# Kernel tuning notes

Hardware: AMD Instinct MI355X
Metric: run time of the kernel (lower is better)

Reference implementation:

```python
import jax, jax.numpy as jnp
import numpy as np

H, NH, NKV, HD, S, B = 4096, 32, 8, 128, 2048, 1
QMAX = 127.0  # int8 symmetric


def fake_quant(x, axis=None):
    """Symmetric int8 fake quantization with straight-through estimator.
    axis=None -> per-tensor dynamic scale; axis=int -> per-channel along that axis."""
    if axis is None:
        amax = jnp.max(jnp.abs(x))
    else:
        amax = jnp.max(jnp.abs(x), axis=axis, keepdims=True)
    scale = jnp.maximum(amax, 1e-8) / QMAX
    q = jnp.clip(jnp.round(x / scale), -QMAX - 1, QMAX) * scale
    return x + jax.lax.stop_gradient(q - x)


def quant_linear(x, w):
    # weight: per-output-channel quant (reduce over in-features axis=1);
    # activation: per-tensor dynamic quant
    xq = fake_quant(x)
    wq = fake_quant(w, axis=1)
    return jnp.einsum('bsh,oh->bso', xq, wq)


def rotate_half(x):
    x1, x2 = jnp.split(x, 2, axis=-1)
    return jnp.concatenate([-x2, x1], axis=-1)


def apply_rope(q, k, cos, sin):
    # q: [B,NH,S,HD], k: [B,NKV,S,HD], cos/sin: [B,S,HD]
    cos = cos[:, None, :, :]
    sin = sin[:, None, :, :]
    return q * cos + rotate_half(q) * sin, k * cos + rotate_half(k) * sin


def setup_inputs() -> dict:
    key = jax.random.key(0)
    ks = jax.random.split(key, 6)
    hidden_states = jax.random.normal(ks[0], (B, S, H), jnp.float32)
    # additive causal mask
    neg = jnp.finfo(jnp.float32).min
    mask = jnp.where(jnp.tril(jnp.ones((S, S), bool)), 0.0, neg)
    attention_mask = jnp.broadcast_to(mask, (B, 1, S, S)).astype(jnp.float32)
    # rotary cos/sin
    inv_freq = 1.0 / (10000.0 ** (jnp.arange(0, HD, 2, dtype=jnp.float32) / HD))
    t = jnp.arange(S, dtype=jnp.float32)
    freqs = jnp.outer(t, inv_freq)                     # [S, HD/2]
    emb = jnp.concatenate([freqs, freqs], axis=-1)     # [S, HD]
    cos = jnp.broadcast_to(jnp.cos(emb), (B, S, HD))
    sin = jnp.broadcast_to(jnp.sin(emb), (B, S, HD))
    sc = 0.02
    wq = jax.random.normal(ks[1], (H, H), jnp.float32) * sc
    wk = jax.random.normal(ks[2], (NKV * HD, H), jnp.float32) * sc
    wv = jax.random.normal(ks[3], (NKV * HD, H), jnp.float32) * sc
    wo = jax.random.normal(ks[4], (H, H), jnp.float32) * sc
    return {"hidden_states": hidden_states, "attention_mask": attention_mask,
            "cos": cos, "sin": sin, "wq": wq, "wk": wk, "wv": wv, "wo": wo}


def reference(hidden_states, attention_mask, cos, sin, wq, wk, wv, wo):
    b, s, _ = hidden_states.shape
    scaling = HD ** -0.5
    q = quant_linear(hidden_states, wq).reshape(b, s, NH, HD).transpose(0, 2, 1, 3)
    k = quant_linear(hidden_states, wk).reshape(b, s, NKV, HD).transpose(0, 2, 1, 3)
    v = quant_linear(hidden_states, wv).reshape(b, s, NKV, HD).transpose(0, 2, 1, 3)
    q, k = apply_rope(q, k, cos, sin)
    groups = NH // NKV
    k = jnp.repeat(k, groups, axis=1)  # [B,NH,S,HD]
    v = jnp.repeat(v, groups, axis=1)
    # quantize before QK^T
    qq = fake_quant(q)
    kq = fake_quant(k)
    attn = jnp.einsum('bhqd,bhkd->bhqk', qq, kq) * scaling
    attn = attn + attention_mask
    attn = jnp.maximum(attn, jnp.finfo(attn.dtype).min)
    attn = jax.nn.softmax(attn.astype(jnp.float32), axis=-1).astype(q.dtype)
    # quantize before PV
    pq = fake_quant(attn)
    vq = fake_quant(v)
    out = jnp.einsum('bhqk,bhkd->bhqd', pq, vq)
    out = out.transpose(0, 2, 1, 3).reshape(b, s, NH * HD)
    out = quant_linear(out, wo)
    return out
```

## Files before the change

### kernel.cpp

```cpp
#include <hip/hip_runtime.h>
#include <cstdint>
#include <cstddef>


#define S_LEN   2048
#define HDIM    4096
#define NHEADS  32
#define NKVH    8
#define HEADD   128
#define QMAXF   127.0f
#define ROPE_BLOCKS 20480

typedef _Float16 half8  __attribute__((ext_vector_type(8)));
typedef _Float16 half2v __attribute__((ext_vector_type(2)));
typedef float    floatx4 __attribute__((ext_vector_type(4)));

__device__ __forceinline__ float wave_max64(float v){
#pragma unroll
  for (int off = 32; off > 0; off >>= 1) v = fmaxf(v, __shfl_xor(v, off));
  return v;
}
__device__ __forceinline__ float quad_max(float v){
  v = fmaxf(v, __shfl_xor(v, 16));
  v = fmaxf(v, __shfl_xor(v, 32));
  return v;
}
__device__ __forceinline__ float quad_sum(float v){
  v += __shfl_xor(v, 16);
  v += __shfl_xor(v, 32);
  return v;
}
__device__ __forceinline__ void atomic_max_f(unsigned* p, float v){
  atomicMax(p, __float_as_uint(v));
}
__device__ __forceinline__ float q8(float x, float scale){
  return fminf(fmaxf(rintf(x / scale), -128.f), 127.f);
}
__device__ __forceinline__ void gload_lds16(const _Float16* g, _Float16* l){
  __builtin_amdgcn_global_load_lds((const __attribute__((address_space(1))) void*)g,
                                   (__attribute__((address_space(3))) void*)l, 16, 0, 0);
}

__device__ __forceinline__ void block_atomic_max(float m, unsigned* out){
  m = wave_max64(m);
  __shared__ float red[4];
  int wid = threadIdx.x >> 6;
  if ((threadIdx.x & 63) == 0) red[wid] = m;
  __syncthreads();
  if (threadIdx.x == 0)
    atomic_max_f(out, fmaxf(fmaxf(red[0], red[1]), fmaxf(red[2], red[3])));
}

__global__ void k_init(float* scal){ if (threadIdx.x < 16) scal[threadIdx.x] = 0.0f; }

__global__ void k_amax(const float* __restrict__ x, size_t n4, unsigned* __restrict__ out){
  size_t i = (size_t)blockIdx.x * blockDim.x + threadIdx.x;
  size_t stride = (size_t)gridDim.x * blockDim.x;
  float m = 0.f;
  for (; i < n4; i += stride){
    float4 v = ((const float4*)x)[i];
    m = fmaxf(m, fmaxf(fmaxf(fabsf(v.x), fabsf(v.y)), fmaxf(fabsf(v.z), fabsf(v.w))));
  }
  block_atomic_max(m, out);
}

__global__ void k_amax_v(const float* __restrict__ Y, unsigned* __restrict__ out){
  size_t i = (size_t)blockIdx.x * blockDim.x + threadIdx.x;
  size_t stride = (size_t)gridDim.x * blockDim.x;
  float m = 0.f;
  for (size_t e = i; e < (size_t)S_LEN * 1024; e += stride){
    size_t s = e >> 10; int c = (int)(e & 1023);
    m = fmaxf(m, fabsf(Y[s * 6144 + 5120 + c]));
  }
  block_atomic_max(m, out);
}

__global__ void k_quant(const float* __restrict__ x, _Float16* __restrict__ q,
                        size_t n4, const float* __restrict__ amax){
  float scale = fmaxf(*amax, 1e-8f) / QMAXF;
  size_t i = (size_t)blockIdx.x * blockDim.x + threadIdx.x;
  size_t stride = (size_t)gridDim.x * blockDim.x;
  for (; i < n4; i += stride){
    float4 v = ((const float4*)x)[i];
    union { _Float16 h[4]; uint2 u; } pk;
    pk.h[0] = (_Float16)q8(v.x, scale);
    pk.h[1] = (_Float16)q8(v.y, scale);
    pk.h[2] = (_Float16)q8(v.z, scale);
    pk.h[3] = (_Float16)q8(v.w, scale);
    ((uint2*)q)[i] = pk.u;
  }
}

__global__ __launch_bounds__(256) void k_quant_w(
    const float* __restrict__ wq, const float* __restrict__ wk,
    const float* __restrict__ wv, const float* __restrict__ wo,
    _Float16* __restrict__ Wall, _Float16* __restrict__ Wo,
    float* __restrict__ wsc)
{
  int row = blockIdx.x;
  const float* src; _Float16* dst;
  if (row < 4096)      { src = wq + (size_t)row * HDIM;          dst = Wall + (size_t)row * HDIM; }
  else if (row < 5120) { src = wk + (size_t)(row - 4096) * HDIM; dst = Wall + (size_t)row * HDIM; }
  else if (row < 6144) { src = wv + (size_t)(row - 5120) * HDIM; dst = Wall + (size_t)row * HDIM; }
  else                 { src = wo + (size_t)(row - 6144) * HDIM; dst = Wo + (size_t)(row - 6144) * HDIM; }
  float4 v[4]; float m = 0.f;
#pragma unroll
  for (int i = 0; i < 4; i++){
    v[i] = ((const float4*)src)[threadIdx.x + i * 256];
    m = fmaxf(m, fmaxf(fmaxf(fabsf(v[i].x), fabsf(v[i].y)), fmaxf(fabsf(v[i].z), fabsf(v[i].w))));
  }
  m = wave_max64(m);
  __shared__ float red[4];
  int wid = threadIdx.x >> 6;
  if ((threadIdx.x & 63) == 0) red[wid] = m;
  __syncthreads();
  float am = fmaxf(fmaxf(red[0], red[1]), fmaxf(red[2], red[3]));
  float scale = fmaxf(am, 1e-8f) / QMAXF;
  if (threadIdx.x == 0) wsc[row] = scale;
#pragma unroll
  for (int i = 0; i < 4; i++){
    union { _Float16 h[4]; uint2 u; } pk;
    pk.h[0] = (_Float16)q8(v[i].x, scale);
    pk.h[1] = (_Float16)q8(v[i].y, scale);
    pk.h[2] = (_Float16)q8(v[i].z, scale);
    pk.h[3] = (_Float16)q8(v[i].w, scale);
    ((uint2*)dst)[threadIdx.x + i * 256] = pk.u;
  }
}

__global__ __launch_bounds__(256) void k_rope(
    float* __restrict__ Y, const float* __restrict__ cosb,
    const float* __restrict__ sinb,
    float* __restrict__ qpart, float* __restrict__ kpart)
{
  int idx = blockIdx.x * 256 + threadIdx.x;
  int s = idx / (40 * 64);
  int rem = idx - s * 40 * 64;
  int head = rem >> 6;
  int d = rem & 63;
  size_t base = (size_t)s * 6144 + (head < 32 ? head * 128 : 4096 + (head - 32) * 128);
  float x1 = Y[base + d], x2 = Y[base + d + 64];
  float c1 = cosb[s * 128 + d],      s1 = sinb[s * 128 + d];
  float c2 = cosb[s * 128 + d + 64], s2 = sinb[s * 128 + d + 64];
  float o1 = x1 * c1 - x2 * s1;
  float o2 = x2 * c2 + x1 * s2;
  Y[base + d] = o1; Y[base + d + 64] = o2;
  float m = wave_max64(fmaxf(fabsf(o1), fabsf(o2)));
  __shared__ float wmax[4]; __shared__ int wisq[4];
  int wid = threadIdx.x >> 6;
  if ((threadIdx.x & 63) == 0){ wmax[wid] = m; wisq[wid] = (head < 32); }
  __syncthreads();
  if (threadIdx.x == 0){
    float qm = 0.f, km = 0.f;
#pragma unroll
    for (int w = 0; w < 4; w++){
      if (wisq[w]) qm = fmaxf(qm, wmax[w]); else km = fmaxf(km, wmax[w]);
    }
    qpart[blockIdx.x] = qm; kpart[blockIdx.x] = km;
  }
}

__global__ __launch_bounds__(256) void k_reduce_qk(
    const float* __restrict__ qpart, const float* __restrict__ kpart,
    float* __restrict__ scal)
{
  const float* src = blockIdx.x ? kpart : qpart;
  float m = 0.f;
  for (int i = threadIdx.x; i < ROPE_BLOCKS; i += 256) m = fmaxf(m, src[i]);
  m = wave_max64(m);
  __shared__ float red[4];
  int wid = threadIdx.x >> 6;
  if ((threadIdx.x & 63) == 0) red[wid] = m;
  __syncthreads();
  if (threadIdx.x == 0)
    scal[1 + blockIdx.x] = fmaxf(fmaxf(red[0], red[1]), fmaxf(red[2], red[3]));
}

__global__ __launch_bounds__(256) void k_quant_qk(
    const float* __restrict__ Y, _Float16* __restrict__ Qh,
    _Float16* __restrict__ Kh, const float* __restrict__ scal)
{
  int i = blockIdx.x * 256 + threadIdx.x;
  int s = i / 1280, c4 = i - s * 1280;
  int col = c4 * 4;
  float4 v = *(const float4*)(Y + (size_t)s * 6144 + col);
  float scale = fmaxf(col < 4096 ? scal[1] : scal[2], 1e-8f) / QMAXF;
  union { _Float16 h[4]; uint2 u; } pk;
  pk.h[0] = (_Float16)q8(v.x, scale);
  pk.h[1] = (_Float16)q8(v.y, scale);
  pk.h[2] = (_Float16)q8(v.z, scale);
  pk.h[3] = (_Float16)q8(v.w, scale);
  if (col < 4096) *(uint2*)(Qh + (size_t)s * 4096 + col) = pk.u;
  else            *(uint2*)(Kh + (size_t)s * 1024 + (col - 4096)) = pk.u;
}

__global__ __launch_bounds__(256) void k_quant_vt(
    const float* __restrict__ Y, _Float16* __restrict__ Vt,
    const float* __restrict__ scal)
{
  __shared__ _Float16 sT[64][72];
  const int s0 = blockIdx.x * 64, kvh = blockIdx.y, dh = blockIdx.z;
  const float scale = fmaxf(scal[3], 1e-8f) / QMAXF;
  const int d = threadIdx.x & 63, srow = threadIdx.x >> 6;
#pragma unroll
  for (int i = 0; i < 16; i++){
    int s = srow + i * 4;
    float v = Y[(size_t)(s0 + s) * 6144 + 5120 + kvh * 128 + dh * 64 + d];
    sT[d][s] = (_Float16)q8(v, scale);
  }
  __syncthreads();
  const int dr = threadIdx.x >> 2, j = threadIdx.x & 3;
  _Float16* dst = Vt + (size_t)kvh * HEADD * S_LEN + (size_t)(dh * 64 + dr) * S_LEN + s0 + j * 16;
  *(uint4*)(dst)     = *(const uint4*)(&sT[dr][j * 16]);
  *(uint4*)(dst + 8) = *(const uint4*)(&sT[dr][j * 16 + 8]);
}

__global__ __launch_bounds__(256) void k_gemm_nt(
    const _Float16* __restrict__ A, const _Float16* __restrict__ B,
    const float* __restrict__ amax_a, const float* __restrict__ sb,
    float* __restrict__ C, int M, int N, int K)
{
  __shared__ _Float16 sA[128 * 32];
  __shared__ _Float16 sB[128 * 32];
  const int m0 = blockIdx.x * 128;
  const int n0 = blockIdx.y * 128;
  const int tid = threadIdx.x;
  const int w = tid >> 6, lane = tid & 63;
  const int quad = lane >> 4, l16 = lane & 15;
  const int wm = (w & 1) * 64, wn = (w >> 1) * 64;
  floatx4 acc[4][4] = {};
  const int srow = w * 16 + (lane >> 2);
  const int scol = (lane & 3) * 8;
  const _Float16* gA0 = A + (size_t)(m0 + srow) * K + scol;
  const _Float16* gA1 = A + (size_t)(m0 + 64 + srow) * K + scol;
  const _Float16* gB0 = B + (size_t)(n0 + srow) * K + scol;
  const _Float16* gB1 = B + (size_t)(n0 + 64 + srow) * K + scol;
  _Float16* dA0 = sA + w * 512 + lane * 8;
  _Float16* dA1 = sA + 2048 + w * 512 + lane * 8;
  _Float16* dB0 = sB + w * 512 + lane * 8;
  _Float16* dB1 = sB + 2048 + w * 512 + lane * 8;

  for (int k0 = 0; k0 < K; k0 += 32){
    __syncthreads();
    gload_lds16(gA0 + k0, dA0);
    gload_lds16(gA1 + k0, dA1);
    gload_lds16(gB0 + k0, dB0);
    gload_lds16(gB1 + k0, dB1);
    __syncthreads();
    half8 af[4], bf[4];
#pragma unroll
    for (int i = 0; i < 4; i++){
      af[i] = *(const half8*)(sA + (wm + i * 16 + l16) * 32 + quad * 8);
      bf[i] = *(const half8*)(sB + (wn + i * 16 + l16) * 32 + quad * 8);
    }
#pragma unroll
    for (int i = 0; i < 4; i++)
#pragma unroll
      for (int j = 0; j < 4; j++)
        acc[i][j] = __builtin_amdgcn_mfma_f32_16x16x32_f16(af[i], bf[j], acc[i][j], 0, 0, 0);
  }
  const float sa = fmaxf(*amax_a, 1e-8f) / QMAXF;
#pragma unroll
  for (int i = 0; i < 4; i++){
    int row = m0 + wm + i * 16 + quad * 4;
#pragma unroll
    for (int j = 0; j < 4; j++){
      int col = n0 + wn + j * 16 + l16;
      float sc2 = sa * sb[col];
#pragma unroll
      for (int rr = 0; rr < 4; rr++)
        C[(size_t)(row + rr) * N + col] = acc[i][j][rr] * sc2;
    }
  }
}

__global__ __launch_bounds__(256, 2) void k_attn(
    const _Float16* __restrict__ Qh,
    const _Float16* __restrict__ Kh,
    const _Float16* __restrict__ Vt,
    const float* __restrict__ scal,
    float* __restrict__ AO)
{
  const int pair = blockIdx.x;
  const int h    = blockIdx.y;
  const int kvh  = h >> 2;
  const int tid  = threadIdx.x;
  const int wid  = tid >> 6, lane = tid & 63;
  const int quad = lane >> 4, l16 = lane & 15;

  __shared__ _Float16 sK[2][8192];
  __shared__ _Float16 sV[2][8192];

  const float s_q = fmaxf(scal[1], 1e-8f) / QMAXF;
  const float s_k = fmaxf(scal[2], 1e-8f) / QMAXF;
  const float s_v = fmaxf(scal[3], 1e-8f) / QMAXF;
  const float qkscale = s_q * s_k * 0.08838834764831845f;
  const float osc = s_v * (1.0f / QMAXF);

  const int srow7 = (wid * 4 + quad) & 7;
  const int sch   = (l16 & 8) | ((l16 ^ srow7) & 7);
  const _Float16* gKs = Kh + (size_t)(wid * 4 + quad) * 1024 + (size_t)kvh * 128 + sch * 8;
  const int vrg = lane >> 3, vp = lane & 7;
  const _Float16* gVs = Vt + (size_t)kvh * (HEADD * S_LEN)
                           + (size_t)(wid * 8 + vrg) * S_LEN + ((vp ^ vrg) & 7) * 8;

  int krd[4];
#pragma unroll
  for (int kk = 0; kk < 4; kk++){
    int c = kk * 4 + quad;
    krd[kk] = l16 * 128 + ((c & 8) | ((c ^ (l16 & 7)) & 7)) * 8;
  }
  const int vrd0 = l16 * 64 + ((quad       ^ (l16 & 7)) & 7) * 8;
  const int vrd1 = l16 * 64 + (((quad ^ 4) ^ (l16 & 7)) & 7) * 8;

  const int sl0 = l16 + 32 * (quad & 1);
  const int sl1 = sl0 + 16;

  auto stage_k = [&](int kt, int buf){
    const _Float16* g = gKs + (size_t)kt * 65536;
    _Float16* d = sK[buf] + wid * 512;
    gload_lds16(g,          d);
    gload_lds16(g + 16384,  d + 2048);
    gload_lds16(g + 32768,  d + 4096);
    gload_lds16(g + 49152,  d + 6144);
  };
  auto stage_v = [&](int kt, int buf){
    const _Float16* g = gVs + (size_t)kt * 64;
    _Float16* d = sV[buf] + wid * 512;
    gload_lds16(g,          d);
    gload_lds16(g + 65536,  d + 2048);
    gload_lds16(g + 131072, d + 4096);
    gload_lds16(g + 196608, d + 6144);
  };

  for (int half = 0; half < 2; half++){
    const int qb = half ? (31 - pair) : pair;
    const int ql = qb * 64 + wid * 16 + l16;
    half8 qf[4];
#pragma unroll
    for (int kk = 0; kk < 4; kk++)
      qf[kk] = *(const half8*)(Qh + (size_t)ql * 4096 + h * 128 + kk * 32 + quad * 8);

    float m = -__builtin_inff(), l = 0.f;

    stage_k(0, 0);
    __syncthreads();
    for (int kt = 0; kt <= qb; ++kt){
      if (kt < qb) stage_k(kt + 1, (kt + 1) & 1);
      const _Float16* kb = sK[kt & 1];
      const bool diag = (kt == qb);
      float s[4][4];
      __builtin_amdgcn_s_setprio(1);
#pragma unroll
      for (int nt = 0; nt < 4; nt++){
        floatx4 c = {};
#pragma unroll
        for (int kk = 0; kk < 4; kk++){
          half8 kf = *(const half8*)(kb + nt * 2048 + krd[kk]);
          c = __builtin_amdgcn_mfma_f32_16x16x32_f16(kf, qf[kk], c, 0, 0, 0);
        }
#pragma unroll
        for (int rr = 0; rr < 4; rr++){
          int kpos = kt * 64 + nt * 16 + quad * 4 + rr;
          float v = c[rr] * qkscale;
          s[nt][rr] = (diag && kpos > ql) ? -__builtin_inff() : v;
        }
      }
      __builtin_amdgcn_s_setprio(0);
      float tm = s[0][0];
#pragma unroll
      for (int nt = 0; nt < 4; nt++)
#pragma unroll
        for (int rr = 0; rr < 4; rr++) tm = fmaxf(tm, s[nt][rr]);
      tm = quad_max(tm);
      float mnew = fmaxf(m, tm);
      float ls = 0.f;
#pragma unroll
      for (int nt = 0; nt < 4; nt++)
#pragma unroll
        for (int rr = 0; rr < 4; rr++) ls += __expf(s[nt][rr] - mnew);
      ls = quad_sum(ls);
      l = l * __expf(m - mnew) + ls;
      m = mnew;
      __syncthreads();
    }
    const float il = QMAXF * __builtin_amdgcn_rcpf(l);

    floatx4 accO[8] = {};
    stage_k(0, 0); stage_v(0, 0);
    __syncthreads();
    for (int kt = 0; kt <= qb; ++kt){
      if (kt < qb){ stage_k(kt + 1, (kt + 1) & 1); stage_v(kt + 1, (kt + 1) & 1); }
      const _Float16* kb = sK[kt & 1];
      const _Float16* vb = sV[kt & 1];
      const bool diag = (kt == qb);
      float p[4][4];
      __builtin_amdgcn_s_setprio(1);
#pragma unroll
      for (int nt = 0; nt < 4; nt++){
        floatx4 c = {};
#pragma unroll
        for (int kk = 0; kk < 4; kk++){
          half8 kf = *(const half8*)(kb + nt * 2048 + krd[kk]);
          c = __builtin_amdgcn_mfma_f32_16x16x32_f16(kf, qf[kk], c, 0, 0, 0);
        }
#pragma unroll
        for (int rr = 0; rr < 4; rr++) p[nt][rr] = c[rr];
      }
      __builtin_amdgcn_s_setprio(0);
      unsigned ph[4][2];
#pragma unroll
      for (int nt = 0; nt < 4; nt++){
        float pq[4];
#pragma unroll
        for (int rr = 0; rr < 4; rr++){
          int kpos = kt * 64 + nt * 16 + quad * 4 + rr;
          float v = fminf(rintf(__expf(p[nt][rr] * qkscale - m) * il), 127.f);
          pq[rr] = (diag && kpos > ql) ? 0.f : v;
        }
        ph[nt][0] = __builtin_bit_cast(unsigned, __builtin_amdgcn_cvt_pkrtz(pq[0], pq[1]));
        ph[nt][1] = __builtin_bit_cast(unsigned, __builtin_amdgcn_cvt_pkrtz(pq[2], pq[3]));
      }
      half8 pb[2];
      const bool hi = (quad >= 2);
#pragma unroll
      for (int ks = 0; ks < 2; ks++){
        unsigned wa0 = __shfl((int)ph[2 * ks][0],     sl0);
        unsigned wb0 = __shfl((int)ph[2 * ks + 1][0], sl0);
        unsigned wa1 = __shfl((int)ph[2 * ks][1],     sl0);
        unsigned wb1 = __shfl((int)ph[2 * ks + 1][1], sl0);
        unsigned wa2 = __shfl((int)ph[2 * ks][0],     sl1);
        unsigned wb2 = __shfl((int)ph[2 * ks + 1][0], sl1);
        unsigned wa3 = __shfl((int)ph[2 * ks][1],     sl1);
        unsigned wb3 = __shfl((int)ph[2 * ks + 1][1], sl1);
        union { unsigned w[4]; half8 v; } u;
        u.w[0] = hi ? wb0 : wa0;
        u.w[1] = hi ? wb1 : wa1;
        u.w[2] = hi ? wb2 : wa2;
        u.w[3] = hi ? wb3 : wa3;
        pb[ks] = u.v;
      }
      __builtin_amdgcn_s_setprio(1);
#pragma unroll
      for (int dt = 0; dt < 8; dt++){
        half8 v0 = *(const half8*)(vb + dt * 1024 + vrd0);
        half8 v1 = *(const half8*)(vb + dt * 1024 + vrd1);
        accO[dt] = __builtin_amdgcn_mfma_f32_16x16x32_f16(v0, pb[0], accO[dt], 0, 0, 0);
        accO[dt] = __builtin_amdgcn_mfma_f32_16x16x32_f16(v1, pb[1], accO[dt], 0, 0, 0);
      }
      __builtin_amdgcn_s_setprio(0);
      __syncthreads();
    }

#pragma unroll
    for (int dt = 0; dt < 8; dt++){
      float4 o;
      o.x = accO[dt][0] * osc; o.y = accO[dt][1] * osc;
      o.z = accO[dt][2] * osc; o.w = accO[dt][3] * osc;
      *(float4*)(AO + (size_t)ql * 4096 + h * 128 + dt * 16 + quad * 4) = o;
    }
  }
}

extern "C" void kernel_launch(void* const* d_in, const int* in_sizes, int n_in,
                              void* d_out, int out_size, void* d_ws, size_t ws_size,
                              hipStream_t stream)
{
  const float* hidden = (const float*)d_in[0];
  const float* cosb = (const float*)d_in[2];
  const float* sinb = (const float*)d_in[3];
  const float* wq = (const float*)d_in[4];
  const float* wk = (const float*)d_in[5];
  const float* wv = (const float*)d_in[6];
  const float* wo = (const float*)d_in[7];
  float* out = (float*)d_out;

  char* ws = (char*)d_ws;
  size_t off = 0;
  auto alloc = [&](size_t bytes){ size_t o = off; off += (bytes + 255) & ~(size_t)255; return o; };
  float*    scal  = (float*)   (ws + alloc(64));
  float*    wsc   = (float*)   (ws + alloc(10240 * 4));
  float*    qpart = (float*)   (ws + alloc(ROPE_BLOCKS * 4));
  float*    kpart = (float*)   (ws + alloc(ROPE_BLOCKS * 4));
  _Float16* Wall  = (_Float16*)(ws + alloc((size_t)6144 * 4096 * 2));
  _Float16* Wo    = (_Float16*)(ws + alloc((size_t)4096 * 4096 * 2));
  _Float16* Xq    = (_Float16*)(ws + alloc((size_t)2048 * 4096 * 2));
  float*    Y     = (float*)   (ws + alloc((size_t)2048 * 6144 * 4));
  _Float16* Qh  = Xq;
  _Float16* Kh  = Wall;
  _Float16* Vt  = Wall + (size_t)2048 * 1024;
  float*    AO  = Y;
  _Float16* AOq = (_Float16*)((char*)Y + (size_t)2048 * 4096 * 4);

  unsigned* su = (unsigned*)scal;

  k_init<<<dim3(1), dim3(64), 0, stream>>>(scal);
  k_quant_w<<<dim3(10240), dim3(256), 0, stream>>>(wq, wk, wv, wo, Wall, Wo, wsc);
  k_amax<<<dim3(256), dim3(256), 0, stream>>>(hidden, (size_t)(2048 * 4096 / 4), su + 0);
  k_quant<<<dim3(2048), dim3(256), 0, stream>>>(hidden, Xq, (size_t)(2048 * 4096 / 4), scal + 0);
  k_gemm_nt<<<dim3(16, 48), dim3(256), 0, stream>>>(Xq, Wall, scal + 0, wsc, Y, 2048, 6144, 4096);
  k_rope<<<dim3(ROPE_BLOCKS), dim3(256), 0, stream>>>(Y, cosb, sinb, qpart, kpart);
  k_reduce_qk<<<dim3(2), dim3(256), 0, stream>>>(qpart, kpart, scal);
  k_amax_v<<<dim3(256), dim3(256), 0, stream>>>(Y, su + 3);
  k_quant_qk<<<dim3(10240), dim3(256), 0, stream>>>(Y, Qh, Kh, scal);
  k_quant_vt<<<dim3(32, 8, 2), dim3(256), 0, stream>>>(Y, Vt, scal);
  k_attn<<<dim3(16, 32), dim3(256), 0, stream>>>(Qh, Kh, Vt, scal, AO);
  k_amax<<<dim3(256), dim3(256), 0, stream>>>(AO, (size_t)(2048 * 4096 / 4), su + 4);
  k_quant<<<dim3(2048), dim3(256), 0, stream>>>(AO, AOq, (size_t)(2048 * 4096 / 4), scal + 4);
  k_gemm_nt<<<dim3(16, 32), dim3(256), 0, stream>>>(AOq, Wo, scal + 4, wsc + 6144, out, 2048, 4096, 4096);
}
```

Before: 651.8 us.

## Double-buffer GEMM with BK=64 swizzled LDS and XCD-aware block remapping

Rewrites the NT GEMM main loop to use two LDS buffers of 128x64 tiles, loaded through an XOR-swizzled layout with async global-to-LDS copies and explicit vmcnt waits. The next tile is prefetched while MFMAs run on the current one, replacing the single-buffer loop that synchronised twice per 32-wide k step. The GEMM and attention grids are remapped so consecutive blocks scheduled on the same XCD share operand tiles for L2 reuse. The GEMM also gains a two-blocks-per-SIMD launch bound, and its doubled LDS footprint may cap occupancy. The remap hardcodes 16 M-tiles, and the attention remap hardcodes the grid dimensions.

```diff
diff --git a/kernel.cpp b/kernel.cpp
--- a/kernel.cpp
+++ b/kernel.cpp
@@ -12,7 +12,6 @@
 #define ROPE_BLOCKS 20480
 
 typedef _Float16 half8  __attribute__((ext_vector_type(8)));
-typedef _Float16 half2v __attribute__((ext_vector_type(2)));
 typedef float    floatx4 __attribute__((ext_vector_type(4)));
 
 __device__ __forceinline__ float wave_max64(float v){
@@ -215,50 +214,89 @@
   *(uint4*)(dst + 8) = *(const uint4*)(&sT[dr][j * 16 + 8]);
 }
 
-__global__ __launch_bounds__(256) void k_gemm_nt(
+__global__ __launch_bounds__(256, 2) void k_gemm_nt(
     const _Float16* __restrict__ A, const _Float16* __restrict__ B,
     const float* __restrict__ amax_a, const float* __restrict__ sb,
     float* __restrict__ C, int M, int N, int K)
 {
-  __shared__ _Float16 sA[128 * 32];
-  __shared__ _Float16 sB[128 * 32];
-  const int m0 = blockIdx.x * 128;
-  const int n0 = blockIdx.y * 128;
+  __shared__ _Float16 sA[2][8192];
+  __shared__ _Float16 sB[2][8192];
+
+  const int nwg  = 16 * gridDim.y;
+  const int orig = blockIdx.x + 16 * blockIdx.y;
+  const int wg   = (orig & 7) * (nwg >> 3) + (orig >> 3);
+  const int m0 = (wg & 15) * 128;
+  const int n0 = (wg >> 4) * 128;
+
   const int tid = threadIdx.x;
   const int w = tid >> 6, lane = tid & 63;
   const int quad = lane >> 4, l16 = lane & 15;
   const int wm = (w & 1) * 64, wn = (w >> 1) * 64;
   floatx4 acc[4][4] = {};
-  const int srow = w * 16 + (lane >> 2);
-  const int scol = (lane & 3) * 8;
-  const _Float16* gA0 = A + (size_t)(m0 + srow) * K + scol;
-  const _Float16* gA1 = A + (size_t)(m0 + 64 + srow) * K + scol;
-  const _Float16* gB0 = B + (size_t)(n0 + srow) * K + scol;
-  const _Float16* gB1 = B + (size_t)(n0 + 64 + srow) * K + scol;
-  _Float16* dA0 = sA + w * 512 + lane * 8;
-  _Float16* dA1 = sA + 2048 + w * 512 + lane * 8;
-  _Float16* dB0 = sB + w * 512 + lane * 8;
-  _Float16* dB1 = sB + 2048 + w * 512 + lane * 8;
-
-  for (int k0 = 0; k0 < K; k0 += 32){
-    __syncthreads();
-    gload_lds16(gA0 + k0, dA0);
-    gload_lds16(gA1 + k0, dA1);
-    gload_lds16(gB0 + k0, dB0);
-    gload_lds16(gB1 + k0, dB1);
-    __syncthreads();
-    half8 af[4], bf[4];
+
+  const int strow = tid >> 3;
+  const int stchk = (tid & 7) ^ (strow & 7);
+  const _Float16* gA = A + (size_t)(m0 + strow) * K + stchk * 8;
+  const _Float16* gB = B + (size_t)(n0 + strow) * K + stchk * 8;
+
+  int offA[4][2], offB[4][2];
+#pragma unroll
+  for (int i = 0; i < 4; i++)
+#pragma unroll
+    for (int kk = 0; kk < 2; kk++){
+      int c = kk * 4 + quad;
+      offA[i][kk] = (wm + i * 16 + l16) * 64 + (c ^ (l16 & 7)) * 8;
+      offB[i][kk] = (wn + i * 16 + l16) * 64 + (c ^ (l16 & 7)) * 8;
+    }
+
+  auto stage = [&](int kt, int buf){
+    const _Float16* a = gA + (size_t)kt * 64;
+    const _Float16* b = gB + (size_t)kt * 64;
+    _Float16* dA = sA[buf] + w * 512;
+    _Float16* dB = sB[buf] + w * 512;
 #pragma unroll
     for (int i = 0; i < 4; i++){
-      af[i] = *(const half8*)(sA + (wm + i * 16 + l16) * 32 + quad * 8);
-      bf[i] = *(const half8*)(sB + (wn + i * 16 + l16) * 32 + quad * 8);
-    }
+      gload_lds16(a + (size_t)i * 32 * K, dA + i * 2048);
+      gload_lds16(b + (size_t)i * 32 * K, dB + i * 2048);
+    }
+  };
+
+  const int NT = K >> 6;
+  stage(0, 0);
+  stage(1, 1);
+  asm volatile("s_waitcnt vmcnt(8)" ::: "memory");
+  __builtin_amdgcn_s_barrier();
+
+  for (int t = 0; t < NT; ++t){
+    const _Float16* a = sA[t & 1];
+    const _Float16* b = sB[t & 1];
+    half8 af[4][2], bf[4][2];
 #pragma unroll
     for (int i = 0; i < 4; i++)
 #pragma unroll
-      for (int j = 0; j < 4; j++)
-        acc[i][j] = __builtin_amdgcn_mfma_f32_16x16x32_f16(af[i], bf[j], acc[i][j], 0, 0, 0);
-  }
+      for (int kk = 0; kk < 2; kk++){
+        af[i][kk] = *(const half8*)(a + offA[i][kk]);
+        bf[i][kk] = *(const half8*)(b + offB[i][kk]);
+      }
+#pragma unroll
+    for (int kk = 0; kk < 2; kk++)
+#pragma unroll
+      for (int i = 0; i < 4; i++)
+#pragma unroll
+        for (int j = 0; j < 4; j++)
+          acc[i][j] = __builtin_amdgcn_mfma_f32_16x16x32_f16(af[i][kk], bf[j][kk], acc[i][j], 0, 0, 0);
+    asm volatile("" ::: "memory");
+    __builtin_amdgcn_s_barrier();
+    if (t + 2 < NT){
+      stage(t + 2, t & 1);
+      asm volatile("s_waitcnt vmcnt(8)" ::: "memory");
+    } else {
+      asm volatile("s_waitcnt vmcnt(0)" ::: "memory");
+    }
+    __builtin_amdgcn_s_barrier();
+    asm volatile("" ::: "memory");
+  }
+
   const float sa = fmaxf(*amax_a, 1e-8f) / QMAXF;
 #pragma unroll
   for (int i = 0; i < 4; i++){
@@ -281,8 +319,10 @@
     const float* __restrict__ scal,
     float* __restrict__ AO)
 {
-  const int pair = blockIdx.x;
-  const int h    = blockIdx.y;
+  const int orig = blockIdx.x + 16 * blockIdx.y;
+  const int wg   = (orig & 7) * 64 + (orig >> 3);
+  const int pair = wg & 15;
+  const int h    = wg >> 4;
   const int kvh  = h >> 2;
   const int tid  = threadIdx.x;
   const int wid  = tid >> 6, lane = tid & 63;
```

Result: no change. 644.1 us (-1.2%).
